# Kernel tuning notes

Measured on AMD Instinct MI355X. Metric: run time of the kernel, lower is better.

The kernel has to match this reference:

```python
import jax, jax.numpy as jnp
import numpy as np

B, T, D, H = 2, 2048, 1024, 16
HD = D // H  # head_dim = 64


def setup_inputs() -> dict:
    key = jax.random.key(0)
    ks = jax.random.split(key, 6)
    s = 1.0 / np.sqrt(D)
    return {
        "x": jax.random.normal(ks[0], (B, T, D), dtype=jnp.float32),
        "Wk": jax.random.uniform(ks[1], (D, D), jnp.float32, -s, s),
        "Wq": jax.random.uniform(ks[2], (D, D), jnp.float32, -s, s),
        "Wv": jax.random.uniform(ks[3], (D, D), jnp.float32, -s, s),
        "Wp": jax.random.uniform(ks[4], (D, D), jnp.float32, -s, s),
        "bp": jax.random.uniform(ks[5], (D,), jnp.float32, -s, s),
    }


def reference(x, Wk, Wq, Wv, Wp, bp):
    Bx, Tx, C = x.shape
    # torch Linear: y = x @ W.T ; split heads -> [B, H, T, HD]
    def split(y):
        return y.reshape(Bx, Tx, H, HD).transpose(0, 2, 1, 3)
    k = split(x @ Wk.T)
    q = split(x @ Wq.T)
    v = split(x @ Wv.T)
    scale = HD ** -0.5
    att = jnp.einsum('bhqd,bhkd->bhqk', q, k) * scale  # [B,H,T,T]
    causal = jnp.tril(jnp.ones((Tx, Tx), dtype=bool))
    att = jnp.where(causal, att, -jnp.inf)
    att = jax.nn.softmax(att, axis=-1)
    out = jnp.einsum('bhqk,bhkd->bhqd', att, v)
    out = out.transpose(0, 2, 1, 3).reshape(Bx, Tx, C)
    return out @ Wp.T + bp
```

## Files before the change

### kernel.cpp

```cpp
#include <hip/hip_runtime.h>

typedef unsigned short u16;
typedef __bf16 bf16;
typedef bf16  bf16x8 __attribute__((ext_vector_type(8)));
typedef float f32x4  __attribute__((ext_vector_type(4)));

constexpr int Bc  = 2;
constexpr int Tc  = 2048;
constexpr int Dc  = 1024;
constexpr int Hc  = 16;
constexpr int HDc = 64;
constexpr int Mg  = Bc * Tc;
constexpr int Kg  = Dc;

__device__ inline u16 f2b(float f) {
    union { float f; unsigned u; } c; c.f = f;
    unsigned r = c.u + 0x7FFFu + ((c.u >> 16) & 1u);
    return (u16)(r >> 16);
}

__device__ inline float exp2_hw(float x) {
    float r; asm("v_exp_f32 %0, %1" : "=v"(r) : "v"(x)); return r;
}
__device__ inline unsigned cvt_pk(float a, float b) {
    unsigned r; asm("v_cvt_pk_bf16_f32 %0, %1, %2" : "=v"(r) : "v"(a), "v"(b)); return r;
}
__device__ inline void gload16(const u16* g, u16* l) {
    __builtin_amdgcn_global_load_lds(
        (const __attribute__((address_space(1))) void*)g,
        (__attribute__((address_space(3))) void*)l, 16, 0, 0);
}

struct CvtArgs { const float* src[5]; u16* dst[5]; int n[5]; };

__global__ __launch_bounds__(256) void cvt_all(CvtArgs a) {
    const int tid = blockIdx.x * blockDim.x + threadIdx.x;
    const int stride = gridDim.x * blockDim.x * 4;
    #pragma unroll
    for (int r = 0; r < 5; ++r) {
        const float* s = a.src[r];
        u16* d = a.dst[r];
        const int n = a.n[r];
        for (int i = tid * 4; i < n; i += stride) {
            float4 v = *reinterpret_cast<const float4*>(s + i);
            ushort4 o;
            o.x = f2b(v.x); o.y = f2b(v.y); o.z = f2b(v.z); o.w = f2b(v.w);
            *reinterpret_cast<ushort4*>(d + i) = o;
        }
    }
}

template<int EPI>
__global__ __launch_bounds__(256) void gemm_bt(
    const u16* __restrict__ A,
    const u16* __restrict__ W0, const u16* __restrict__ W1, const u16* __restrict__ W2,
    u16* __restrict__ dQ, u16* __restrict__ dK, u16* __restrict__ dV,
    const float* __restrict__ bias, float* __restrict__ outF)
{
    __shared__ u16 As[128 * 32];
    __shared__ u16 Bs[128 * 32];

    const int t    = threadIdx.x;
    const int z    = blockIdx.z;
    const int m0   = blockIdx.y * 128;
    const int n0   = blockIdx.x * 128;
    const u16* Wsel = (z == 0) ? W0 : (z == 1) ? W1 : W2;

    const int lane = t & 63, wave = t >> 6;
    const int wm = wave >> 1, wn = wave & 1;
    const int lo = lane & 15, hi = lane >> 4;

    f32x4 acc[4][4];
    const f32x4 fzero = {0.f, 0.f, 0.f, 0.f};
    #pragma unroll
    for (int i = 0; i < 4; ++i)
        #pragma unroll
        for (int j = 0; j < 4; ++j) acc[i][j] = fzero;

    const int rA = t >> 2;
    const int ks = ((t & 3) ^ (rA & 3)) * 8;
    const u16* gA0 = A    + (size_t)(m0 + rA) * Kg + ks;
    const u16* gA1 = gA0 + 64 * Kg;
    const u16* gB0 = Wsel + (size_t)(n0 + rA) * Kg + ks;
    const u16* gB1 = gB0 + 64 * Kg;
    u16* lA0 = &As[(wave * 16) * 32];
    u16* lA1 = &As[(64 + wave * 16) * 32];
    u16* lB0 = &Bs[(wave * 16) * 32];
    u16* lB1 = &Bs[(64 + wave * 16) * 32];

    const int sl = (hi ^ (lo & 3)) * 8;

    for (int k0 = 0; k0 < Kg; k0 += 32) {
        __syncthreads();
        gload16(gA0 + k0, lA0);
        gload16(gA1 + k0, lA1);
        gload16(gB0 + k0, lB0);
        gload16(gB1 + k0, lB1);
        __syncthreads();

        bf16x8 af[4], bfr[4];
        #pragma unroll
        for (int fi = 0; fi < 4; ++fi)
            af[fi] = *reinterpret_cast<const bf16x8*>(&As[(wm * 64 + fi * 16 + lo) * 32 + sl]);
        #pragma unroll
        for (int fj = 0; fj < 4; ++fj)
            bfr[fj] = *reinterpret_cast<const bf16x8*>(&Bs[(wn * 64 + fj * 16 + lo) * 32 + sl]);
        #pragma unroll
        for (int fi = 0; fi < 4; ++fi)
            #pragma unroll
            for (int fj = 0; fj < 4; ++fj)
                acc[fi][fj] = __builtin_amdgcn_mfma_f32_16x16x32_bf16(af[fi], bfr[fj], acc[fi][fj], 0, 0, 0);
    }

    #pragma unroll
    for (int fi = 0; fi < 4; ++fi) {
        #pragma unroll
        for (int fj = 0; fj < 4; ++fj) {
            const int nn = n0 + wn * 64 + fj * 16 + lo;
            if constexpr (EPI == 0) {
                const int b = m0 >> 11;
                const int h = nn >> 6, hd = nn & 63;
                if (z == 2) {
                    const int tt0 = (m0 & (Tc - 1)) + wm * 64 + fi * 16 + hi * 4;
                    const int tile = tt0 >> 6;
                    const int k6   = tt0 & 63;
                    const int slot = ((k6 & 32) >> 3) + ((k6 & 15) >> 2);
                    const int halfE = (k6 & 16) >> 2;
                    const size_t off =
                        (((size_t)(b * Hc + h) * 32 + tile) * 64 + hd) * 64 + slot * 8 + halfE;
                    ushort4 pv;
                    pv.x = f2b(acc[fi][fj][0]); pv.y = f2b(acc[fi][fj][1]);
                    pv.z = f2b(acc[fi][fj][2]); pv.w = f2b(acc[fi][fj][3]);
                    *reinterpret_cast<ushort4*>(&dV[off]) = pv;
                } else {
                    u16* dst = (z == 0) ? dQ : dK;
                    #pragma unroll
                    for (int r = 0; r < 4; ++r) {
                        const int m = m0 + wm * 64 + fi * 16 + hi * 4 + r;
                        const int tt = m & (Tc - 1);
                        dst[((((b * Hc + h) << 11) + tt) * HDc) + hd] = f2b(acc[fi][fj][r]);
                    }
                }
            } else {
                #pragma unroll
                for (int r = 0; r < 4; ++r) {
                    const int m = m0 + wm * 64 + fi * 16 + hi * 4 + r;
                    outF[(size_t)m * Dc + nn] = acc[fi][fj][r] + bias[nn];
                }
            }
        }
    }
}

__global__ __launch_bounds__(512, 4) void attn_kernel(const u16* __restrict__ Q,
                                                      const u16* __restrict__ Kk,
                                                      const u16* __restrict__ Vp,
                                                      u16* __restrict__ O)
{
    __shared__ u16 Kl[2][64][64];
    __shared__ u16 Vl[2][64][64];
    float* Ob = (float*)&Kl[0][0][0];
    float* Mb = (float*)&Vl[0][0][0];
    float* Lb = Mb + 64;

    const int t = threadIdx.x;
    const int w = t >> 6;
    const int lane = t & 63;
    const int j = w >> 1, c = w & 1;
    const int lo = lane & 15, hi = lane >> 4;
    const int l8 = lane >> 3, l7 = lane & 7;
    const int bi = blockIdx.x;
    const int bh = blockIdx.y;
    const int p  = bi + 16 * j;
    const int ql0 = 16 * p;
    const int qh0 = 16 * (127 - p);
    const int NT  = ((2047 - 16 * bi) >> 6) + 1;

    const u16* Qp = Q  + (size_t)bh * Tc * HDc;
    const u16* Kp = Kk + (size_t)bh * Tc * HDc;
    const u16* Vq = Vp + (size_t)bh * Tc * HDc;

    const float sc2 = 0.125f * 1.44269504f;
    const f32x4 fzero = {0.f, 0.f, 0.f, 0.f};

    bf16x8 qfl[2], qfh[2];
    #pragma unroll
    for (int h = 0; h < 2; ++h) {
        union { bf16x8 v; u16 u[8]; } a2, r2;
        a2.v = *reinterpret_cast<const bf16x8*>(Qp + (ql0 + lo) * HDc + 32 * h + 8 * hi);
        #pragma unroll
        for (int jj = 0; jj < 8; ++jj) {
            union { float f; unsigned u; } cc; cc.u = ((unsigned)a2.u[jj]) << 16;
            r2.u[jj] = f2b(cc.f * sc2);
        }
        qfl[h] = r2.v;
        a2.v = *reinterpret_cast<const bf16x8*>(Qp + (qh0 + lo) * HDc + 32 * h + 8 * hi);
        #pragma unroll
        for (int jj = 0; jj < 8; ++jj) {
            union { float f; unsigned u; } cc; cc.u = ((unsigned)a2.u[jj]) << 16;
            r2.u[jj] = f2b(cc.f * sc2);
        }
        qfh[h] = r2.v;
    }

    f32x4 ol[4], oh[4];
    float ml = -__builtin_inff(), mh = -__builtin_inff();
    float ll = 0.f, lh = 0.f;
    #pragma unroll
    for (int d = 0; d < 4; ++d) { ol[d] = fzero; oh[d] = fzero; }

    const int rb = 8 * w;
    const int swz = (l7 ^ l8) * 8;
    auto stage = [&](int tile, int b) {
        const u16* ksrc = Kp + (size_t)(tile * 64 + rb + l8) * 64 + swz;
        const u16* vsrc = Vq + (size_t)(tile * 64 + rb + l8) * 64 + swz;
        gload16(ksrc, &Kl[b][rb][0]);
        gload16(vsrc, &Vl[b][rb][0]);
    };

    auto step16 = [&](int kb, int q0v, const bf16x8 (&qv)[2], f32x4 (&o)[4],
                      float& m2, float& l2,
                      const bf16x8 (&kf)[2][2], const bf16x8 (&vf)[4]) {
        f32x4 s0, s1;
        s0 = __builtin_amdgcn_mfma_f32_16x16x32_bf16(kf[0][0], qv[0], fzero, 0, 0, 0);
        s0 = __builtin_amdgcn_mfma_f32_16x16x32_bf16(kf[0][1], qv[1], s0, 0, 0, 0);
        s1 = __builtin_amdgcn_mfma_f32_16x16x32_bf16(kf[1][0], qv[0], fzero, 0, 0, 0);
        s1 = __builtin_amdgcn_mfma_f32_16x16x32_bf16(kf[1][1], qv[1], s1, 0, 0, 0);

        if (kb + 31 > q0v) {
            const int q = q0v + lo;
            #pragma unroll
            for (int r = 0; r < 4; ++r) {
                if (kb + 4 * hi + r > q)      s0[r] = -__builtin_inff();
                if (kb + 16 + 4 * hi + r > q) s1[r] = -__builtin_inff();
            }
        }

        const float lmax = fmaxf(
            fmaxf(fmaxf(s0[0], s0[1]), fmaxf(s0[2], s0[3])),
            fmaxf(fmaxf(s1[0], s1[1]), fmaxf(s1[2], s1[3])));

        if (!__all(lmax <= m2 + 11.5f)) {
            float tmx = lmax;
            tmx = fmaxf(tmx, __shfl_xor(tmx, 16));
            tmx = fmaxf(tmx, __shfl_xor(tmx, 32));
            const float mn = fmaxf(m2, tmx);
            const float aq = exp2_hw(m2 - mn);
            m2 = mn;
            l2 *= aq;
            float ar[4];
            #pragma unroll
            for (int r = 0; r < 4; ++r) ar[r] = __shfl(aq, 4 * hi + r);
            #pragma unroll
            for (int d = 0; d < 4; ++d)
                #pragma unroll
                for (int r = 0; r < 4; ++r) o[d][r] *= ar[r];
        }

        float pr[8];
        #pragma unroll
        for (int r = 0; r < 4; ++r) pr[r]     = exp2_hw(s0[r] - m2);
        #pragma unroll
        for (int r = 0; r < 4; ++r) pr[4 + r] = exp2_hw(s1[r] - m2);
        l2 += ((pr[0] + pr[1]) + (pr[2] + pr[3])) + ((pr[4] + pr[5]) + (pr[6] + pr[7]));
        union { bf16x8 v; unsigned wv[4]; } pk;
        pk.wv[0] = cvt_pk(pr[0], pr[1]);
        pk.wv[1] = cvt_pk(pr[2], pr[3]);
        pk.wv[2] = cvt_pk(pr[4], pr[5]);
        pk.wv[3] = cvt_pk(pr[6], pr[7]);
        #pragma unroll
        for (int d = 0; d < 4; ++d)
            o[d] = __builtin_amdgcn_mfma_f32_16x16x32_bf16(pk.v, vf[d], o[d], 0, 0, 0);
    };

    stage(0, 0);
    __syncthreads();

    for (int tt = 0; tt < NT; ++tt) {
        const int cur = tt & 1;
        if (tt + 1 < NT) stage(tt + 1, cur ^ 1);
        const int kb = (tt << 6) + 32 * c;

        const bool hAct = (kb <= qh0 + 15);
        const bool lAct = (kb <= ql0 + 15);
        if (hAct || lAct) {
            const int sw = lo & 7;
            bf16x8 kf[2][2];
            #pragma unroll
            for (int kt = 0; kt < 2; ++kt)
                #pragma unroll
                for (int h = 0; h < 2; ++h)
                    kf[kt][h] = *reinterpret_cast<const bf16x8*>(
                        &Kl[cur][32 * c + 16 * kt + lo][((4 * h + hi) ^ sw) * 8]);
            bf16x8 vf[4];
            #pragma unroll
            for (int d = 0; d < 4; ++d)
                vf[d] = *reinterpret_cast<const bf16x8*>(
                    &Vl[cur][16 * d + lo][((4 * c + hi) ^ sw) * 8]);

            if (hAct) step16(kb, qh0, qfh, oh, mh, lh, kf, vf);
            if (lAct) step16(kb, ql0, qfl, ol, ml, ll, kf, vf);
        }
        __syncthreads();
    }

    const int b = bh >> 4, h = bh & 15;
    #pragma unroll
    for (int ph = 0; ph < 2; ++ph) {
        const f32x4* om = (ph == 0) ? oh : ol;
        const float  mm = (ph == 0) ? mh : ml;
        const float  lm = (ph == 0) ? lh : ll;
        const int    q0 = (ph == 0) ? qh0 : ql0;

        if (c == 1) {
            float lt = lm;
            lt += __shfl_xor(lt, 16);
            lt += __shfl_xor(lt, 32);
            if (hi == 0) { Mb[j * 16 + lo] = mm; Lb[j * 16 + lo] = lt; }
            float* op = Ob + (j * 64 + lane) * 16;
            #pragma unroll
            for (int d = 0; d < 4; ++d)
                #pragma unroll
                for (int r = 0; r < 4; ++r) op[d * 4 + r] = om[d][r];
        }
        __syncthreads();
        if (c == 0) {
            float lt = lm;
            lt += __shfl_xor(lt, 16);
            lt += __shfl_xor(lt, 32);
            const float m1 = Mb[j * 16 + lo];
            const float l1 = Lb[j * 16 + lo];
            const float M  = fmaxf(mm, m1);
            const float e0 = exp2_hw(mm - M);
            const float e1 = exp2_hw(m1 - M);
            const float Li = 1.0f / (lt * e0 + l1 * e1);
            float e0r[4], e1r[4], Lir[4];
            #pragma unroll
            for (int r = 0; r < 4; ++r) {
                e0r[r] = __shfl(e0, 4 * hi + r);
                e1r[r] = __shfl(e1, 4 * hi + r);
                Lir[r] = __shfl(Li, 4 * hi + r);
            }
            const float* op = Ob + (j * 64 + lane) * 16;
            #pragma unroll
            for (int d = 0; d < 4; ++d)
                #pragma unroll
                for (int r = 0; r < 4; ++r) {
                    const int q = q0 + 4 * hi + r;
                    const float val = (om[d][r] * e0r[r] + op[d * 4 + r] * e1r[r]) * Lir[r];
                    O[(size_t)(b * Tc + q) * Dc + h * 64 + 16 * d + lo] = f2b(val);
                }
        }
        __syncthreads();
    }
}

extern "C" void kernel_launch(void* const* d_in, const int* in_sizes, int n_in,
                              void* d_out, int out_size, void* d_ws, size_t ws_size,
                              hipStream_t stream) {
    (void)in_sizes; (void)n_in; (void)out_size; (void)ws_size;
    const float* x  = (const float*)d_in[0];
    const float* Wk = (const float*)d_in[1];
    const float* Wq = (const float*)d_in[2];
    const float* Wv = (const float*)d_in[3];
    const float* Wp = (const float*)d_in[4];
    const float* bp = (const float*)d_in[5];
    float* out = (float*)d_out;

    char* ws = (char*)d_ws;
    u16* xb   = (u16*)(ws);
    u16* wqb  = (u16*)(ws + (8u  << 20));
    u16* wkb  = (u16*)(ws + (10u << 20));
    u16* wvb  = (u16*)(ws + (12u << 20));
    u16* wpb  = (u16*)(ws + (14u << 20));
    u16* Qb   = (u16*)(ws + (16u << 20));
    u16* Kb   = (u16*)(ws + (24u << 20));
    u16* Vtb  = (u16*)(ws + (32u << 20));
    u16* attb = (u16*)(ws + (40u << 20));

    CvtArgs ca;
    ca.src[0] = x;  ca.dst[0] = xb;  ca.n[0] = Mg * Dc;
    ca.src[1] = Wq; ca.dst[1] = wqb; ca.n[1] = Dc * Dc;
    ca.src[2] = Wk; ca.dst[2] = wkb; ca.n[2] = Dc * Dc;
    ca.src[3] = Wv; ca.dst[3] = wvb; ca.n[3] = Dc * Dc;
    ca.src[4] = Wp; ca.dst[4] = wpb; ca.n[4] = Dc * Dc;
    cvt_all<<<dim3(1024), 256, 0, stream>>>(ca);

    gemm_bt<0><<<dim3(Dc / 128, Mg / 128, 3), 256, 0, stream>>>(
        xb, wqb, wkb, wvb, Qb, Kb, Vtb, nullptr, nullptr);

    attn_kernel<<<dim3(16, Bc * Hc), 512, 0, stream>>>(Qb, Kb, Vtb, attb);

    gemm_bt<1><<<dim3(Dc / 128, Mg / 128, 1), 256, 0, stream>>>(
        attb, wpb, wpb, wpb, nullptr, nullptr, nullptr, bp, out);
}
```

Measured before the change: 110.3 us.

## Split attention KV work across four waves per query tile and retune GEMM swizzle

The attention kernel now assigns four waves to each pair of query tiles instead of two. Each wave takes one 32-key half of every other 64-key tile, the grid doubles to 32 blocks per head, and the epilogue merges three partial softmax states through shared memory. The aim is more parallelism and occupancy on the causal attention. The cost is extra merge work, a larger staging buffer, and duplicated tile staging per block. A tighter launch bound may also force register spills. Separately, the GEMM LDS XOR swizzle now keys on row pairs, meant to cut bank conflicts on the 64-byte rows.

```diff
diff --git a/kernel.cpp b/kernel.cpp
--- a/kernel.cpp
+++ b/kernel.cpp
@@ -78,7 +78,7 @@
         for (int j = 0; j < 4; ++j) acc[i][j] = fzero;
 
     const int rA = t >> 2;
-    const int ks = ((t & 3) ^ (rA & 3)) * 8;
+    const int ks = ((t & 3) ^ ((rA >> 1) & 3)) * 8;
     const u16* gA0 = A    + (size_t)(m0 + rA) * Kg + ks;
     const u16* gA1 = gA0 + 64 * Kg;
     const u16* gB0 = Wsel + (size_t)(n0 + rA) * Kg + ks;
@@ -88,7 +88,7 @@
     u16* lB0 = &Bs[(wave * 16) * 32];
     u16* lB1 = &Bs[(64 + wave * 16) * 32];
 
-    const int sl = (hi ^ (lo & 3)) * 8;
+    const int sl = (hi ^ ((lo >> 1) & 3)) * 8;
 
     for (int k0 = 0; k0 < Kg; k0 += 32) {
         __syncthreads();
@@ -152,26 +152,27 @@
     }
 }
 
-__global__ __launch_bounds__(512, 4) void attn_kernel(const u16* __restrict__ Q,
+__global__ __launch_bounds__(512, 8) void attn_kernel(const u16* __restrict__ Q,
                                                       const u16* __restrict__ Kk,
                                                       const u16* __restrict__ Vp,
                                                       u16* __restrict__ O)
 {
-    __shared__ u16 Kl[2][64][64];
-    __shared__ u16 Vl[2][64][64];
-    float* Ob = (float*)&Kl[0][0][0];
-    float* Mb = (float*)&Vl[0][0][0];
-    float* Lb = Mb + 64;
+    __shared__ __align__(16) char smem[32768];
+    u16 (*Kl)[64][64] = (u16(*)[64][64])smem;
+    u16 (*Vl)[64][64] = (u16(*)[64][64])(smem + 16384);
+    float* Ob = (float*)smem;
+    float* Mb = (float*)(smem + 24576);
+    float* Lb = (float*)(smem + 25344);
 
     const int t = threadIdx.x;
     const int w = t >> 6;
     const int lane = t & 63;
-    const int j = w >> 1, c = w & 1;
+    const int j = w >> 2, c = w & 3;
     const int lo = lane & 15, hi = lane >> 4;
     const int l8 = lane >> 3, l7 = lane & 7;
     const int bi = blockIdx.x;
     const int bh = blockIdx.y;
-    const int p  = bi + 16 * j;
+    const int p  = bi + 32 * j;
     const int ql0 = 16 * p;
     const int qh0 = 16 * (127 - p);
     const int NT  = ((2047 - 16 * bi) >> 6) + 1;
@@ -276,30 +277,34 @@
     stage(0, 0);
     __syncthreads();
 
+    const int myHalf = 32 * (c & 1);
+    const int myPar  = c >> 1;
     for (int tt = 0; tt < NT; ++tt) {
         const int cur = tt & 1;
         if (tt + 1 < NT) stage(tt + 1, cur ^ 1);
-        const int kb = (tt << 6) + 32 * c;
-
-        const bool hAct = (kb <= qh0 + 15);
-        const bool lAct = (kb <= ql0 + 15);
-        if (hAct || lAct) {
-            const int sw = lo & 7;
-            bf16x8 kf[2][2];
-            #pragma unroll
-            for (int kt = 0; kt < 2; ++kt)
-                #pragma unroll
-                for (int h = 0; h < 2; ++h)
-                    kf[kt][h] = *reinterpret_cast<const bf16x8*>(
-                        &Kl[cur][32 * c + 16 * kt + lo][((4 * h + hi) ^ sw) * 8]);
-            bf16x8 vf[4];
-            #pragma unroll
-            for (int d = 0; d < 4; ++d)
-                vf[d] = *reinterpret_cast<const bf16x8*>(
-                    &Vl[cur][16 * d + lo][((4 * c + hi) ^ sw) * 8]);
-
-            if (hAct) step16(kb, qh0, qfh, oh, mh, lh, kf, vf);
-            if (lAct) step16(kb, ql0, qfl, ol, ml, ll, kf, vf);
+
+        if ((tt & 1) == myPar) {
+            const int kb = (tt << 6) + myHalf;
+            const bool hAct = (kb <= qh0 + 15);
+            const bool lAct = (kb <= ql0 + 15);
+            if (hAct || lAct) {
+                const int sw = lo & 7;
+                bf16x8 kf[2][2];
+                #pragma unroll
+                for (int kt = 0; kt < 2; ++kt)
+                    #pragma unroll
+                    for (int h = 0; h < 2; ++h)
+                        kf[kt][h] = *reinterpret_cast<const bf16x8*>(
+                            &Kl[cur][myHalf + 16 * kt + lo][((4 * h + hi) ^ sw) * 8]);
+                bf16x8 vf[4];
+                #pragma unroll
+                for (int d = 0; d < 4; ++d)
+                    vf[d] = *reinterpret_cast<const bf16x8*>(
+                        &Vl[cur][16 * d + lo][(((myHalf >> 3) + hi) ^ sw) * 8]);
+
+                if (hAct) step16(kb, qh0, qfh, oh, mh, lh, kf, vf);
+                if (lAct) step16(kb, ql0, qfl, ol, ml, ll, kf, vf);
+            }
         }
         __syncthreads();
     }
@@ -312,12 +317,16 @@
         const float  lm = (ph == 0) ? lh : ll;
         const int    q0 = (ph == 0) ? qh0 : ql0;
 
-        if (c == 1) {
-            float lt = lm;
-            lt += __shfl_xor(lt, 16);
-            lt += __shfl_xor(lt, 32);
-            if (hi == 0) { Mb[j * 16 + lo] = mm; Lb[j * 16 + lo] = lt; }
-            float* op = Ob + (j * 64 + lane) * 16;
+        float lt = lm;
+        lt += __shfl_xor(lt, 16);
+        lt += __shfl_xor(lt, 32);
+
+        if (c != 0) {
+            if (hi == 0) {
+                Mb[(j * 3 + c - 1) * 16 + lo] = mm;
+                Lb[(j * 3 + c - 1) * 16 + lo] = lt;
+            }
+            float* op = Ob + ((j * 3 + c - 1) * 64 + lane) * 16;
             #pragma unroll
             for (int d = 0; d < 4; ++d)
                 #pragma unroll
@@ -325,30 +334,39 @@
         }
         __syncthreads();
         if (c == 0) {
-            float lt = lm;
-            lt += __shfl_xor(lt, 16);
-            lt += __shfl_xor(lt, 32);
-            const float m1 = Mb[j * 16 + lo];
-            const float l1 = Lb[j * 16 + lo];
-            const float M  = fmaxf(mm, m1);
+            float ms[3], ls[3];
+            #pragma unroll
+            for (int s = 0; s < 3; ++s) {
+                ms[s] = Mb[(j * 3 + s) * 16 + lo];
+                ls[s] = Lb[(j * 3 + s) * 16 + lo];
+            }
+            float M = mm;
+            #pragma unroll
+            for (int s = 0; s < 3; ++s) M = fmaxf(M, ms[s]);
             const float e0 = exp2_hw(mm - M);
-            const float e1 = exp2_hw(m1 - M);
-            const float Li = 1.0f / (lt * e0 + l1 * e1);
-            float e0r[4], e1r[4], Lir[4];
+            float es[3];
+            float L = lt * e0;
+            #pragma unroll
+            for (int s = 0; s < 3; ++s) { es[s] = exp2_hw(ms[s] - M); L += ls[s] * es[s]; }
+            const float Li = 1.0f / L;
+            float e0r[4], esr[3][4], Lir[4];
             #pragma unroll
             for (int r = 0; r < 4; ++r) {
                 e0r[r] = __shfl(e0, 4 * hi + r);
-                e1r[r] = __shfl(e1, 4 * hi + r);
                 Lir[r] = __shfl(Li, 4 * hi + r);
-            }
-            const float* op = Ob + (j * 64 + lane) * 16;
+                #pragma unroll
+                for (int s = 0; s < 3; ++s) esr[s][r] = __shfl(es[s], 4 * hi + r);
+            }
             #pragma unroll
             for (int d = 0; d < 4; ++d)
                 #pragma unroll
                 for (int r = 0; r < 4; ++r) {
+                    float acc = om[d][r] * e0r[r];
+                    #pragma unroll
+                    for (int s = 0; s < 3; ++s)
+                        acc += Ob[((j * 3 + s) * 64 + lane) * 16 + d * 4 + r] * esr[s][r];
                     const int q = q0 + 4 * hi + r;
-                    const float val = (om[d][r] * e0r[r] + op[d * 4 + r] * e1r[r]) * Lir[r];
-                    O[(size_t)(b * Tc + q) * Dc + h * 64 + 16 * d + lo] = f2b(val);
+                    O[(size_t)(b * Tc + q) * Dc + h * 64 + 16 * d + lo] = f2b(acc * Lir[r]);
                 }
         }
         __syncthreads();
@@ -389,7 +407,7 @@
     gemm_bt<0><<<dim3(Dc / 128, Mg / 128, 3), 256, 0, stream>>>(
         xb, wqb, wkb, wvb, Qb, Kb, Vtb, nullptr, nullptr);
 
-    attn_kernel<<<dim3(16, Bc * Hc), 512, 0, stream>>>(Qb, Kb, Vtb, attb);
+    attn_kernel<<<dim3(32, Bc * Hc), 512, 0, stream>>>(Qb, Kb, Vtb, attb);
 
     gemm_bt<1><<<dim3(Dc / 128, Mg / 128, 1), 256, 0, stream>>>(
         attb, wpb, wpb, wpb, nullptr, nullptr, nullptr, bp, out);
```

Result: slower. 419.6 us (+280.3%).
